# Kernel tuning notes

Hardware: AMD Instinct MI355X
Metric: run time of the kernel (lower is better)

Reference implementation:

```python
import jax, jax.numpy as jnp
import numpy as np

B = 2
SP = (480, 360, 32)   # spatial_shape (z, y, x)
GS = (8, 8, 8)        # query_gs_ratio
EP = (40, 15, 16)     # embed_params (pool compress ratio)
H = 8
N = 120000
D = 256
OUT = 20


def _dims(rat):
    return tuple((s + r - 1) // r for s, r in zip(SP, rat))


def sine_pe(coords, d_pos):
    # coords: [M,3] float voxel coords in original grid units; normalized sine PE
    nf = d_pos // 6
    sp = jnp.asarray(SP, jnp.float32)
    cn = coords / sp * (2.0 * jnp.pi)                      # normalize=True
    t = 10000.0 ** (jnp.arange(nf, dtype=jnp.float32) / nf)
    ang = cn[:, :, None] / t                               # [M,3,nf]
    pe = jnp.concatenate([jnp.sin(ang), jnp.cos(ang)], -1).reshape(coords.shape[0], -1)
    return jnp.pad(pe, ((0, 0), (0, d_pos - 6 * nf)))


def setup_inputs() -> dict:
    key = jax.random.key(0)
    ks = jax.random.split(key, 24)
    idx_b = jax.random.randint(ks[0], (N, 1), 0, B)
    idx_z = jax.random.randint(ks[1], (N, 1), 0, SP[0])
    idx_y = jax.random.randint(ks[2], (N, 1), 0, SP[1])
    idx_x = jax.random.randint(ks[3], (N, 1), 0, SP[2])
    indices = jnp.concatenate([idx_b, idx_z, idx_y, idx_x], axis=1).astype(jnp.int32)
    s = D ** -0.5
    p = lambda k, sh: jax.random.normal(k, sh, jnp.float32) * s
    return {
        'features': jax.random.normal(ks[4], (N, D), jnp.float32),
        'W_pool': p(ks[5], (D, D)), 'b_pool': jnp.zeros((D,), jnp.float32),
        'W_emb': p(ks[6], (D, D)), 'b_emb': jnp.zeros((D,), jnp.float32),
        'Wq': p(ks[7], (D, D)), 'bq': jnp.zeros((D,), jnp.float32),
        'Wk': p(ks[8], (D, D)), 'bk': jnp.zeros((D,), jnp.float32),
        'Wv': p(ks[9], (D, D)), 'bv': jnp.zeros((D,), jnp.float32),
        'Wo': p(ks[10], (D, D)), 'bo': jnp.zeros((D,), jnp.float32),
        'ln_g': jnp.ones((D,), jnp.float32), 'ln_b': jnp.zeros((D,), jnp.float32),
        'W_seg': p(ks[11], (D, OUT)), 'b_seg': jnp.zeros((OUT,), jnp.float32),
        'indices': indices,
        'batch_size': B,
    }


def reference(features, W_pool, b_pool, W_emb, b_emb, Wq, bq, Wk, bk, Wv, bv,
              Wo, bo, ln_g, ln_b, W_seg, b_seg, indices, batch_size):
    Zd, Yd, Xd = _dims(GS)
    Gq = Zd * Yd * Xd
    Sq = batch_size * Gq
    Ze, Ye, Xe = _dims(EP)
    Gk = Ze * Ye * Xe
    Sk = batch_size * Gk
    n = features.shape[0]

    # --- query pool branch: linear -> voxel-grid scatter_max ---
    pf = features @ W_pool + b_pool                                    # [N,D]
    dq = indices[:, 1:] // jnp.asarray(GS, jnp.int32)
    seg_q = ((indices[:, 0] * Zd + dq[:, 0]) * Yd + dq[:, 1]) * Xd + dq[:, 2]
    pool_max = jax.ops.segment_max(pf, seg_q, num_segments=Sq)
    cnt_q = jax.ops.segment_sum(jnp.ones((n,), jnp.float32), seg_q, num_segments=Sq)
    mq = cnt_q > 0
    pool_max = jnp.where(mq[:, None], pool_max, 0.0)
    cell = jnp.arange(Sq)
    rem = cell % Gq
    pool_c = jnp.stack([(rem // (Yd * Xd)) * GS[0],
                        ((rem // Xd) % Yd) * GS[1],
                        (rem % Xd) * GS[2]], -1).astype(jnp.float32)   # [Sq,3]

    # --- embedding branch ('pool'): linear -> coarse scatter_max + per-channel argmax coords ---
    ef = features @ W_emb + b_emb                                      # [N,D]
    de = indices[:, 1:] // jnp.asarray(EP, jnp.int32)
    seg_k = ((indices[:, 0] * Ze + de[:, 0]) * Ye + de[:, 1]) * Xe + de[:, 2]
    emb_max = jax.ops.segment_max(ef, seg_k, num_segments=Sk)
    cnt_k = jax.ops.segment_sum(jnp.ones((n,), jnp.float32), seg_k, num_segments=Sk)
    mk = cnt_k > 0
    emb_max = jnp.where(mk[:, None], emb_max, 0.0)
    winner = ef == jnp.where(mk[:, None], emb_max, -jnp.inf)[seg_k]
    idx = jax.ops.segment_max(jnp.where(winner, jnp.arange(n)[:, None], -1), seg_k, num_segments=Sk)
    idx_c = jnp.clip(idx, 0, n - 1)                                    # [Sk,D]
    ec = de.astype(jnp.float32)                                        # [N,3] downsampled coords
    emb_c = ec[idx_c].mean(axis=1) * jnp.asarray(EP, jnp.float32)      # [Sk,3]

    # --- position encoding (pointwise sine PE; per-batch loop in torch is pointwise-equivalent) ---
    pool_max = pool_max + sine_pe(pool_c, D)
    emb_max = emb_max + sine_pe(emb_c, D)

    # --- multi-head cross-attention (Q=pool, K/V=embedding), per-batch via dense grid reshape ---
    q_in = pool_max.reshape(batch_size, Gq, D)
    kv_in = emb_max.reshape(batch_size, Gk, D)
    dh = D // H
    q = (q_in @ Wq + bq).reshape(batch_size, Gq, H, dh)
    k = (kv_in @ Wk + bk).reshape(batch_size, Gk, H, dh)
    v = (kv_in @ Wv + bv).reshape(batch_size, Gk, H, dh)
    scores = jnp.einsum('bqhd,bkhd->bhqk', q, k) / jnp.float32(dh) ** 0.5
    kmask = mk.reshape(batch_size, Gk)
    scores = jnp.where(kmask[:, None, None, :], scores, -1e9)
    attn = jax.nn.softmax(scores, axis=-1)
    o = jnp.einsum('bhqk,bkhd->bqhd', attn, v).reshape(batch_size, Gq, D) @ Wo + bo
    h = q_in + o                                                       # residual + LayerNorm sublayer
    mu = h.mean(-1, keepdims=True)
    var = h.var(-1, keepdims=True)
    h = (h - mu) * jax.lax.rsqrt(var + 1e-5) * ln_g + ln_b
    feats_mhca = h.reshape(Sq, D)

    # --- gather back to voxels via pool_inv, residual, seg head (center-tap of SubMConv3d) ---
    vox = features + feats_mhca[seg_q]
    logits = vox @ W_seg + b_seg
    return logits
```

## Files before the change

### kernel.cpp

```cpp
#include <hip/hip_runtime.h>
#include <math.h>

#define N_PTS 120000
#define D 256
#define BATCH 2
#define NH 8
#define DH 32
#define OUTC 20

#define Zd 60
#define Yd 45
#define Xd 4
#define Gq 10800
#define Sq 21600

#define Ze 12
#define Ye 24
#define Xe 2
#define Gk 576
#define Sk 1152

typedef __bf16 bf16_t;
typedef __attribute__((ext_vector_type(8))) __bf16 bf16x8;
typedef __attribute__((ext_vector_type(4))) __bf16 bf16x4;
typedef __attribute__((ext_vector_type(4))) float f32x4;

__device__ __forceinline__ void glds16(const void* g, void* l) {
    __builtin_amdgcn_global_load_lds(
        (const __attribute__((address_space(1))) unsigned int*)g,
        (__attribute__((address_space(3))) unsigned int*)l,
        16, 0, 0);
}

__global__ __launch_bounds__(256) void k_prep(
    const float* __restrict__ Wp, const float* __restrict__ We,
    const float* __restrict__ Wq, const float* __restrict__ Wk,
    const float* __restrict__ Wv, const float* __restrict__ Wo,
    const float* __restrict__ bp, const float* __restrict__ be,
    const float* __restrict__ bk, const float* __restrict__ bv,
    const float* __restrict__ Wseg, const float* __restrict__ bseg,
    bf16_t* __restrict__ Wpe, bf16_t* __restrict__ Wqt,
    bf16_t* __restrict__ Wkv, bf16_t* __restrict__ Wot,
    bf16_t* __restrict__ Wsegt,
    float* __restrict__ bpe, float* __restrict__ bkv,
    float* __restrict__ bsegp)
{
    int n = blockIdx.x, k = threadIdx.x;
    if (n < 512) {
        const float* S = (n < 256) ? Wp : We;
        int nn = n & 255;
        Wpe[n * 256 + k] = (bf16_t)S[k * 256 + nn];
    } else if (n < 768) {
        int nn = n - 512;
        Wqt[nn * 256 + k] = (bf16_t)Wq[k * 256 + nn];
    } else if (n < 1280) {
        int m2 = n - 768;
        const float* S = (m2 < 256) ? Wk : Wv;
        int nn = m2 & 255;
        Wkv[m2 * 256 + k] = (bf16_t)S[k * 256 + nn];
    } else if (n < 1536) {
        int nn = n - 1280;
        Wot[nn * 256 + k] = (bf16_t)Wo[k * 256 + nn];
    } else if (n == 1536) {
        bpe[k] = bp[k]; bpe[256 + k] = be[k];
        bkv[k] = bk[k]; bkv[256 + k] = bv[k];
        if (k < 32) bsegp[k] = (k < OUTC) ? bseg[k] : 0.f;
    } else {
        int n2 = n - 1537;
        Wsegt[n2 * 256 + k] = (n2 < OUTC) ? (bf16_t)Wseg[k * OUTC + n2] : (bf16_t)0.f;
    }
}

__global__ __launch_bounds__(256) void k_cast(
    const float* __restrict__ in, bf16_t* __restrict__ out)
{
    const size_t total = (size_t)N_PTS * 32;
    const size_t stride = (size_t)gridDim.x * 256;
    for (size_t i = (size_t)blockIdx.x * 256 + threadIdx.x; i < total; i += stride) {
        float4 a = *(const float4*)(in + i * 8);
        float4 b = *(const float4*)(in + i * 8 + 4);
        bf16x8 o;
        o[0] = (bf16_t)a.x; o[1] = (bf16_t)a.y; o[2] = (bf16_t)a.z; o[3] = (bf16_t)a.w;
        o[4] = (bf16_t)b.x; o[5] = (bf16_t)b.y; o[6] = (bf16_t)b.z; o[7] = (bf16_t)b.w;
        *(bf16x8*)(out + i * 8) = o;
    }
}

__global__ __launch_bounds__(256) void k_count(
    const int* __restrict__ indices, int* __restrict__ cnt_q, int* __restrict__ cnt_k,
    int* __restrict__ segq, int* __restrict__ segk)
{
    int i = blockIdx.x * 256 + threadIdx.x;
    if (i >= N_PTS) return;
    const int* id = indices + (size_t)i * 4;
    int b = id[0], z = id[1], y = id[2], x = id[3];
    int sq = ((b * Zd + (z >> 3)) * Yd + (y >> 3)) * Xd + (x >> 3);
    int sk = ((b * Ze + (z / 40)) * Ye + (y / 15)) * Xe + (x >> 4);
    segq[i] = sq; segk[i] = sk;
    atomicAdd(&cnt_q[sq], 1);
    atomicAdd(&cnt_k[sk], 1);
}

__global__ __launch_bounds__(1024) void k_scan(
    const int* __restrict__ cnt, int n, int* __restrict__ offs, int* __restrict__ cursor)
{
    __shared__ int wbase[17];
    __shared__ int carry_s;
    const int t = threadIdx.x, lane = t & 63, w = t >> 6;
    if (t == 0) carry_s = 0;
    __syncthreads();
    for (int base = 0; base < n; base += 1024) {
        int v = (base + t < n) ? cnt[base + t] : 0;
        int incl = v;
        #pragma unroll
        for (int off = 1; off < 64; off <<= 1) {
            int u = __shfl_up(incl, off);
            if (lane >= off) incl += u;
        }
        if (lane == 63) wbase[w + 1] = incl;
        __syncthreads();
        if (t == 0) {
            int s = 0;
            wbase[0] = 0;
            #pragma unroll
            for (int i = 1; i <= 16; ++i) { s += wbase[i]; wbase[i] = s; }
        }
        __syncthreads();
        int excl = incl - v + wbase[w] + carry_s;
        if (base + t < n) { offs[base + t] = excl; cursor[base + t] = excl; }
        __syncthreads();
        if (t == 0) carry_s += wbase[16];
        __syncthreads();
    }
}

__global__ __launch_bounds__(256) void k_place(
    const int* __restrict__ segq, const int* __restrict__ segk,
    int* __restrict__ cur_q, int* __restrict__ cur_k,
    int* __restrict__ ids_q, int* __restrict__ ids_k)
{
    int i = blockIdx.x * 256 + threadIdx.x;
    if (i >= N_PTS) return;
    ids_q[atomicAdd(&cur_q[segq[i]], 1)] = i;
    ids_k[atomicAdd(&cur_k[segk[i]], 1)] = i;
}

__global__ __launch_bounds__(256) void k_gemm_bf(
    const bf16_t* __restrict__ A, int M,
    const bf16_t* __restrict__ Wt, const float* __restrict__ bias,
    bf16_t* __restrict__ outb, int ldo)
{
    __shared__ __align__(16) bf16_t Abuf[128 * 64];
    __shared__ __align__(16) bf16_t Bbuf[128 * 64];

    const int t = threadIdx.x;
    const int wave = t >> 6, lane = t & 63;
    const int wr = wave >> 1, wc = wave & 1;
    const int lrow = lane & 15, quad = lane >> 4;
    const int lr8 = lane >> 3, lc8 = lane & 7;
    const int row0 = blockIdx.y * 128;
    const int ntile = blockIdx.x;

    f32x4 acc[4][4];
    #pragma unroll
    for (int mi = 0; mi < 4; ++mi)
        #pragma unroll
        for (int ni = 0; ni < 4; ++ni)
            acc[mi][ni] = (f32x4){0.f, 0.f, 0.f, 0.f};

    for (int k0 = 0; k0 < 256; k0 += 64) {
        #pragma unroll
        for (int i = 0; i < 4; ++i) {
            int chunk = wave * 4 + i;
            int rowA = row0 + chunk * 8 + lr8;
            if (rowA > M - 1) rowA = M - 1;
            glds16(A + (size_t)rowA * 256 + k0 + lc8 * 8, &Abuf[chunk * 512]);
        }
        #pragma unroll
        for (int i = 0; i < 4; ++i) {
            int chunk = wave * 4 + i;
            glds16(Wt + (size_t)(ntile * 128 + chunk * 8 + lr8) * 256 + k0 + lc8 * 8,
                   &Bbuf[chunk * 512]);
        }
        asm volatile("s_waitcnt vmcnt(0)" ::: "memory");
        __builtin_amdgcn_sched_barrier(0);
        __syncthreads();

        #pragma unroll
        for (int kk = 0; kk < 64; kk += 32) {
            bf16x8 Af[4], Bf[4];
            #pragma unroll
            for (int mi = 0; mi < 4; ++mi)
                Af[mi] = *(const bf16x8*)&Abuf[(wr * 64 + mi * 16 + lrow) * 64 + kk + quad * 8];
            #pragma unroll
            for (int ni = 0; ni < 4; ++ni)
                Bf[ni] = *(const bf16x8*)&Bbuf[(wc * 64 + ni * 16 + lrow) * 64 + kk + quad * 8];
            #pragma unroll
            for (int mi = 0; mi < 4; ++mi)
                #pragma unroll
                for (int ni = 0; ni < 4; ++ni)
                    acc[mi][ni] = __builtin_amdgcn_mfma_f32_16x16x32_bf16(
                        Af[mi], Bf[ni], acc[mi][ni], 0, 0, 0);
        }
        __syncthreads();
    }

    const int colb = ntile * 128 + wc * 64;
    float biasv[4];
    #pragma unroll
    for (int ni = 0; ni < 4; ++ni) biasv[ni] = bias[colb + ni * 16 + lrow];

    #pragma unroll
    for (int mi = 0; mi < 4; ++mi) {
        int lr = wr * 64 + mi * 16 + quad * 4;
        #pragma unroll
        for (int reg = 0; reg < 4; ++reg) {
            int grow = row0 + lr + reg;
            if (grow >= M) continue;
            #pragma unroll
            for (int ni = 0; ni < 4; ++ni) {
                int col = colb + ni * 16 + lrow;
                outb[(size_t)grow * ldo + col] = (bf16_t)(acc[mi][ni][reg] + biasv[ni]);
            }
        }
    }
}

__global__ __launch_bounds__(512, 2) void k_gemm(
    const float* __restrict__ A, int M,
    const bf16_t* __restrict__ Wt, const float* __restrict__ bias,
    int mode, float* __restrict__ outp, int ldo)
{
    __shared__ __align__(16) bf16_t Abuf[128][72];
    __shared__ __align__(16) bf16_t Bbuf[256][72];

    const int t = threadIdx.x;
    const int wave = t >> 6, lane = t & 63;
    const int wr = wave >> 2, wc = wave & 3;
    const int lrow = lane & 15, quad = lane >> 4;
    const int row0 = blockIdx.y * 128;
    const int ntile = blockIdx.x;

    f32x4 acc[4][4];
    #pragma unroll
    for (int mi = 0; mi < 4; ++mi)
        #pragma unroll
        for (int ni = 0; ni < 4; ++ni)
            acc[mi][ni] = (f32x4){0.f, 0.f, 0.f, 0.f};

    for (int k0 = 0; k0 < 256; k0 += 64) {
        #pragma unroll
        for (int i = 0; i < 4; ++i) {
            int c = i * 512 + t;
            int r = c >> 4, c4 = c & 15;
            float4 v = make_float4(0.f, 0.f, 0.f, 0.f);
            if (row0 + r < M)
                v = *(const float4*)(A + (size_t)(row0 + r) * 256 + k0 + c4 * 4);
            bf16x4 bv4;
            bv4[0] = (bf16_t)v.x; bv4[1] = (bf16_t)v.y;
            bv4[2] = (bf16_t)v.z; bv4[3] = (bf16_t)v.w;
            *(bf16x4*)&Abuf[r][c4 * 4] = bv4;
        }
        #pragma unroll
        for (int i = 0; i < 4; ++i) {
            int c = i * 512 + t;
            int r = c >> 3, c8 = c & 7;
            uint4 w = *(const uint4*)(Wt + ((size_t)(ntile * 256 + r)) * 256 + k0 + c8 * 8);
            *(uint4*)&Bbuf[r][c8 * 8] = w;
        }
        __syncthreads();

        #pragma unroll
        for (int kk = 0; kk < 64; kk += 32) {
            bf16x8 Af[4], Bf[4];
            #pragma unroll
            for (int mi = 0; mi < 4; ++mi)
                Af[mi] = *(const bf16x8*)&Abuf[wr * 64 + mi * 16 + lrow][kk + quad * 8];
            #pragma unroll
            for (int ni = 0; ni < 4; ++ni)
                Bf[ni] = *(const bf16x8*)&Bbuf[wc * 64 + ni * 16 + lrow][kk + quad * 8];
            #pragma unroll
            for (int mi = 0; mi < 4; ++mi)
                #pragma unroll
                for (int ni = 0; ni < 4; ++ni)
                    acc[mi][ni] = __builtin_amdgcn_mfma_f32_16x16x32_bf16(
                        Af[mi], Bf[ni], acc[mi][ni], 0, 0, 0);
        }
        __syncthreads();
    }

    const int colb = ntile * 256 + wc * 64;
    float biasv[4];
    #pragma unroll
    for (int ni = 0; ni < 4; ++ni) biasv[ni] = bias[colb + ni * 16 + lrow];

    if (mode == 0) {
        #pragma unroll
        for (int mi = 0; mi < 4; ++mi) {
            int lr = wr * 64 + mi * 16 + quad * 4;
            #pragma unroll
            for (int reg = 0; reg < 4; ++reg) {
                int grow = row0 + lr + reg;
                if (grow >= M) continue;
                #pragma unroll
                for (int ni = 0; ni < 4; ++ni) {
                    int col = colb + ni * 16 + lrow;
                    outp[(size_t)grow * ldo + col] = acc[mi][ni][reg] + biasv[ni];
                }
            }
        }
    } else {
        bf16_t* outb = (bf16_t*)outp;
        #pragma unroll
        for (int mi = 0; mi < 4; ++mi) {
            int lr = wr * 64 + mi * 16 + quad * 4;
            #pragma unroll
            for (int reg = 0; reg < 4; ++reg) {
                int grow = row0 + lr + reg;
                if (grow >= M) continue;
                #pragma unroll
                for (int ni = 0; ni < 4; ++ni) {
                    int col = colb + ni * 16 + lrow;
                    outb[(size_t)grow * ldo + col] = (bf16_t)(acc[mi][ni][reg] + biasv[ni]);
                }
            }
        }
    }
}

__device__ inline float pe_val(int j, float cz, float cy, float cx) {
    if (j >= 252) return 0.f;
    int dim = j / 84;
    int f = j % 84;
    int fi = (f >= 42) ? (f - 42) : f;
    float c  = (dim == 0) ? cz : ((dim == 1) ? cy : cx);
    float sp = (dim == 0) ? 480.f : ((dim == 1) ? 360.f : 32.f);
    float cn = c / sp * 6.28318530717958647692f;
    float tt = expf((float)fi * (9.210340371976184f / 42.f));
    float ang = cn / tt;
    return (f >= 42) ? cosf(ang) : sinf(ang);
}

__global__ __launch_bounds__(256) void k_pool_q(
    const bf16_t* __restrict__ pfb, const int* __restrict__ ids,
    const int* __restrict__ offs, const int* __restrict__ cnt,
    float* __restrict__ out)
{
    const int t = threadIdx.x, lane = t & 63, w = t >> 6;
    const int s = blockIdx.x * 4 + w;
    if (s >= Sq) return;
    const int count = cnt[s], start = offs[s];
    float mx[4] = {-3.0e38f, -3.0e38f, -3.0e38f, -3.0e38f};
    for (int r = 0; r < count; ++r) {
        int i = ids[start + r];
        bf16x4 v = *(const bf16x4*)(pfb + (size_t)i * 256 + lane * 4);
        #pragma unroll
        for (int j = 0; j < 4; ++j) mx[j] = fmaxf(mx[j], (float)v[j]);
    }
    int rem = s % Gq;
    float cz = (float)((rem / (Yd * Xd)) * 8);
    float cy = (float)(((rem / Xd) % Yd) * 8);
    float cx = (float)((rem % Xd) * 8);
    #pragma unroll
    for (int j = 0; j < 4; ++j) {
        float v = (count > 0) ? mx[j] : 0.f;
        out[(size_t)s * 256 + lane * 4 + j] = v + pe_val(lane * 4 + j, cz, cy, cx);
    }
}

__global__ __launch_bounds__(512) void k_pool_k(
    const bf16_t* __restrict__ efb, const int* __restrict__ ids,
    const int* __restrict__ offs, const int* __restrict__ cnt,
    float* __restrict__ out, int* __restrict__ kmask)
{
    __shared__ float red[8][256];
    const int t = threadIdx.x, lane = t & 63, w = t >> 6;
    const int s = blockIdx.x;
    const int count = cnt[s], start = offs[s];
    float mx[4] = {-3.0e38f, -3.0e38f, -3.0e38f, -3.0e38f};
    for (int r = w; r < count; r += 8) {
        int i = ids[start + r];
        bf16x4 v = *(const bf16x4*)(efb + (size_t)i * 256 + lane * 4);
        #pragma unroll
        for (int j = 0; j < 4; ++j) mx[j] = fmaxf(mx[j], (float)v[j]);
    }
    #pragma unroll
    for (int j = 0; j < 4; ++j) red[w][lane * 4 + j] = mx[j];
    __syncthreads();
    if (t < 256) {
        float m = red[0][t];
        #pragma unroll
        for (int i = 1; i < 8; ++i) m = fmaxf(m, red[i][t]);
        if (count == 0) m = 0.f;
        int rem = s % Gk;
        float cz = (float)((rem / (Ye * Xe)) * 40);
        float cy = (float)(((rem / Xe) % Ye) * 15);
        float cx = (float)((rem % Xe) * 16);
        out[(size_t)s * 256 + t] = m + pe_val(t, cz, cy, cx);
        if (t == 0) kmask[s] = (count > 0) ? 1 : 0;
    }
}

__global__ __launch_bounds__(256) void k_attn_mfma(
    const bf16_t* __restrict__ Q, const bf16_t* __restrict__ KV,
    const int* __restrict__ kmask, float* __restrict__ O)
{
    __shared__ __align__(16) bf16_t Qs[64][40];
    __shared__ __align__(16) bf16_t Ks[192][40];
    __shared__ __align__(16) bf16_t Vts[32][200];
    __shared__ __align__(16) bf16_t Ps[4][16][200];
    __shared__ float mskf[192];

    const int bh = blockIdx.y;
    const int b = bh >> 3, h = bh & 7;
    const int t = threadIdx.x, wave = t >> 6, lane = t & 63;
    const int lrow = lane & 15, quad = lane >> 4;
    const int q0 = blockIdx.x * 64;

    {
        int r = t >> 2, part = t & 3;
        int qi = q0 + r;
        uint4 val = make_uint4(0u, 0u, 0u, 0u);
        if (qi < Gq)
            val = *(const uint4*)(Q + ((size_t)(b * Gq + qi)) * 256 + h * 32 + part * 8);
        *(uint4*)&Qs[r][part * 8] = val;
    }
    __syncthreads();

    const bf16x8 Aq = *(const bf16x8*)&Qs[wave * 16 + lrow][quad * 8];

    f32x4 oacc[2];
    oacc[0] = (f32x4){0.f, 0.f, 0.f, 0.f};
    oacc[1] = (f32x4){0.f, 0.f, 0.f, 0.f};
    float m_run[4], l_run[4];
    #pragma unroll
    for (int r = 0; r < 4; ++r) { m_run[r] = -3.0e38f; l_run[r] = 0.f; }

    for (int c0 = 0; c0 < Gk; c0 += 192) {
        __syncthreads();
        #pragma unroll
        for (int i = 0; i < 3; ++i) {
            int idx = i * 256 + t;
            int kk = idx >> 2, part = idx & 3;
            uint4 val = *(const uint4*)(KV + ((size_t)(b * Gk + c0 + kk)) * 512 + h * 32 + part * 8);
            *(uint4*)&Ks[kk][part * 8] = val;
        }
        #pragma unroll
        for (int i = 0; i < 3; ++i) {
            int idx = i * 256 + t;
            int kk = idx >> 2, part = idx & 3;
            bf16x8 v = *(const bf16x8*)(KV + ((size_t)(b * Gk + c0 + kk)) * 512 + 256 + h * 32 + part * 8);
            #pragma unroll
            for (int j = 0; j < 8; ++j)
                Vts[part * 8 + j][kk] = v[j];
        }
        if (t < 192) mskf[t] = kmask[b * Gk + c0 + t] ? 0.f : -1.0e9f;
        __syncthreads();

        float sreg[12][4];
        #pragma unroll
        for (int nt = 0; nt < 12; ++nt) {
            bf16x8 Bk = *(const bf16x8*)&Ks[nt * 16 + lrow][quad * 8];
            f32x4 sacc = __builtin_amdgcn_mfma_f32_16x16x32_bf16(
                Aq, Bk, (f32x4){0.f, 0.f, 0.f, 0.f}, 0, 0, 0);
            float pen = mskf[nt * 16 + lrow];
            #pragma unroll
            for (int r = 0; r < 4; ++r)
                sreg[nt][r] = sacc[r] * 0.17677669529663688f + pen;
        }

        float alpha[4];
        #pragma unroll
        for (int r = 0; r < 4; ++r) {
            float mx = sreg[0][r];
            #pragma unroll
            for (int nt = 1; nt < 12; ++nt) mx = fmaxf(mx, sreg[nt][r]);
            #pragma unroll
            for (int off = 1; off < 16; off <<= 1)
                mx = fmaxf(mx, __shfl_xor(mx, off));
            float mnew = fmaxf(m_run[r], mx);
            alpha[r] = __expf(m_run[r] - mnew);
            m_run[r] = mnew;
            l_run[r] *= alpha[r];
        }
        #pragma unroll
        for (int n2 = 0; n2 < 2; ++n2)
            #pragma unroll
            for (int r = 0; r < 4; ++r) oacc[n2][r] *= alpha[r];

        float psum[4] = {0.f, 0.f, 0.f, 0.f};
        #pragma unroll
        for (int nt = 0; nt < 12; ++nt) {
            #pragma unroll
            for (int r = 0; r < 4; ++r) {
                float p = __expf(sreg[nt][r] - m_run[r]);
                psum[r] += p;
                Ps[wave][quad * 4 + r][nt * 16 + lrow] = (bf16_t)p;
            }
        }
        #pragma unroll
        for (int r = 0; r < 4; ++r) {
            float s = psum[r];
            #pragma unroll
            for (int off = 1; off < 16; off <<= 1) s += __shfl_xor(s, off);
            l_run[r] += s;
        }

        #pragma unroll
        for (int ks = 0; ks < 6; ++ks) {
            bf16x8 Ap = *(const bf16x8*)&Ps[wave][lrow][ks * 32 + quad * 8];
            #pragma unroll
            for (int n2 = 0; n2 < 2; ++n2) {
                bf16x8 Bv = *(const bf16x8*)&Vts[n2 * 16 + lrow][ks * 32 + quad * 8];
                oacc[n2] = __builtin_amdgcn_mfma_f32_16x16x32_bf16(
                    Ap, Bv, oacc[n2], 0, 0, 0);
            }
        }
    }

    #pragma unroll
    for (int r = 0; r < 4; ++r) {
        int qi = q0 + wave * 16 + quad * 4 + r;
        if (qi >= Gq) continue;
        float inv = (l_run[r] > 0.f) ? (1.f / l_run[r]) : 0.f;
        #pragma unroll
        for (int n2 = 0; n2 < 2; ++n2)
            O[((size_t)(b * Gq + qi)) * 256 + h * 32 + n2 * 16 + lrow] = oacc[n2][r] * inv;
    }
}

__global__ __launch_bounds__(256) void k_ln(
    const float* __restrict__ oproj, const float* __restrict__ resid,
    const float* __restrict__ g, const float* __restrict__ bta,
    float* __restrict__ out)
{
    const int s = blockIdx.x, t = threadIdx.x;
    float h = resid[(size_t)s * D + t] + oproj[(size_t)s * D + t];

    float s1 = h, s2 = h * h;
    for (int o = 32; o > 0; o >>= 1) {
        s1 += __shfl_down(s1, o);
        s2 += __shfl_down(s2, o);
    }
    __shared__ float r1[4], r2[4];
    __shared__ float mu_s, rstd_s;
    int w = t >> 6;
    if ((t & 63) == 0) { r1[w] = s1; r2[w] = s2; }
    __syncthreads();
    if (t == 0) {
        float a = r1[0] + r1[1] + r1[2] + r1[3];
        float bsum = r2[0] + r2[1] + r2[2] + r2[3];
        float mu = a * (1.f / 256.f);
        float var = bsum * (1.f / 256.f) - mu * mu;
        mu_s = mu;
        rstd_s = rsqrtf(var + 1e-5f);
    }
    __syncthreads();
    out[(size_t)s * D + t] = (h - mu_s) * rstd_s * g[t] + bta[t];
}

__global__ __launch_bounds__(512, 2) void k_logits_mfma(
    const float* __restrict__ feat, const float* __restrict__ mhca,
    const int* __restrict__ indices, const bf16_t* __restrict__ Wsegt,
    const float* __restrict__ bsegp, float* __restrict__ out)
{
    __shared__ __align__(16) bf16_t Abuf[128][72];
    __shared__ __align__(16) bf16_t Bbuf[32][72];
    __shared__ int sq_s[128];

    const int t = threadIdx.x;
    const int wave = t >> 6, lane = t & 63;
    const int lrow = lane & 15, quad = lane >> 4;
    const int row0 = blockIdx.x * 128;

    if (t < 128) {
        int row = row0 + t;
        if (row < N_PTS) {
            const int* id = indices + (size_t)row * 4;
            sq_s[t] = ((id[0] * Zd + (id[1] >> 3)) * Yd + (id[2] >> 3)) * Xd + (id[3] >> 3);
        } else sq_s[t] = 0;
    }
    __syncthreads();

    f32x4 acc[2];
    acc[0] = (f32x4){0.f, 0.f, 0.f, 0.f};
    acc[1] = (f32x4){0.f, 0.f, 0.f, 0.f};

    for (int k0 = 0; k0 < 256; k0 += 64) {
        #pragma unroll
        for (int i = 0; i < 4; ++i) {
            int c = i * 512 + t;
            int r = c >> 4, c4 = c & 15;
            float4 v = make_float4(0.f, 0.f, 0.f, 0.f);
            int grow = row0 + r;
            if (grow < N_PTS) {
                v = *(const float4*)(feat + (size_t)grow * 256 + k0 + c4 * 4);
                float4 m = *(const float4*)(mhca + (size_t)sq_s[r] * 256 + k0 + c4 * 4);
                v.x += m.x; v.y += m.y; v.z += m.z; v.w += m.w;
            }
            bf16x4 bv4;
            bv4[0] = (bf16_t)v.x; bv4[1] = (bf16_t)v.y;
            bv4[2] = (bf16_t)v.z; bv4[3] = (bf16_t)v.w;
            *(bf16x4*)&Abuf[r][c4 * 4] = bv4;
        }
        if (t < 256) {
            int r = t >> 3, c8 = t & 7;
            uint4 w = *(const uint4*)(Wsegt + (size_t)r * 256 + k0 + c8 * 8);
            *(uint4*)&Bbuf[r][c8 * 8] = w;
        }
        __syncthreads();

        #pragma unroll
        for (int kk = 0; kk < 64; kk += 32) {
            bf16x8 Af = *(const bf16x8*)&Abuf[wave * 16 + lrow][kk + quad * 8];
            #pragma unroll
            for (int ni = 0; ni < 2; ++ni) {
                bf16x8 Bf = *(const bf16x8*)&Bbuf[ni * 16 + lrow][kk + quad * 8];
                acc[ni] = __builtin_amdgcn_mfma_f32_16x16x32_bf16(
                    Af, Bf, acc[ni], 0, 0, 0);
            }
        }
        __syncthreads();
    }

    #pragma unroll
    for (int ni = 0; ni < 2; ++ni) {
        int col = ni * 16 + lrow;
        if (col >= OUTC) continue;
        float bias = bsegp[col];
        #pragma unroll
        for (int reg = 0; reg < 4; ++reg) {
            int grow = row0 + wave * 16 + quad * 4 + reg;
            if (grow >= N_PTS) continue;
            out[(size_t)grow * OUTC + col] = acc[ni][reg] + bias;
        }
    }
}

extern "C" void kernel_launch(void* const* d_in, const int* in_sizes, int n_in,
                              void* d_out, int out_size, void* d_ws, size_t ws_size,
                              hipStream_t stream) {
    const float* features = (const float*)d_in[0];
    const float* W_pool = (const float*)d_in[1];
    const float* b_pool = (const float*)d_in[2];
    const float* W_emb  = (const float*)d_in[3];
    const float* b_emb  = (const float*)d_in[4];
    const float* Wq = (const float*)d_in[5];
    const float* bq = (const float*)d_in[6];
    const float* Wk = (const float*)d_in[7];
    const float* bk = (const float*)d_in[8];
    const float* Wv = (const float*)d_in[9];
    const float* bv = (const float*)d_in[10];
    const float* Wo = (const float*)d_in[11];
    const float* bo = (const float*)d_in[12];
    const float* ln_g = (const float*)d_in[13];
    const float* ln_b = (const float*)d_in[14];
    const float* W_seg = (const float*)d_in[15];
    const float* b_seg = (const float*)d_in[16];
    const int* indices = (const int*)d_in[17];
    float* out = (float*)d_out;

    float* ws = (float*)d_ws;
    const size_t SQD = (size_t)Sq * D;
    const size_t SKD = (size_t)Sk * D;
    const size_t PFB_FL = (size_t)N_PTS * D / 2;

    size_t oP   = 0;
    size_t oPF  = oP + PFB_FL;
    size_t oEF  = oPF + SQD;
    size_t oWpe = oEF + SKD;
    size_t oWqt = oWpe + 65536;
    size_t oWkv = oWqt + 32768;
    size_t oWot = oWkv + 65536;
    size_t obpe = oWot + 32768;
    size_t obkv = obpe + 512;
    size_t oCnt = obkv + 512;
    size_t oOffq = oCnt + 21600 + 1152;
    size_t oCurq = oOffq + 21600;
    size_t oOffk = oCurq + 21600;
    size_t oCurk = oOffk + 1152;
    size_t oSegq = oCurk + 1152;
    size_t oSegk = oSegq + N_PTS;
    size_t oIdsq = oSegk + N_PTS;
    size_t oIdsk = oIdsq + N_PTS;
    size_t oKm   = oIdsk + N_PTS;
    size_t oWst  = oKm + 1152;
    size_t obsg  = oWst + 4096;
    size_t oFB   = obsg + 32;

    bf16_t* pfb = (bf16_t*)(ws + oP);
    float* pool_feat = ws + oPF;
    float* emb_feat  = ws + oEF;
    bf16_t* Wpe = (bf16_t*)(ws + oWpe);
    bf16_t* Wqt = (bf16_t*)(ws + oWqt);
    bf16_t* Wkv = (bf16_t*)(ws + oWkv);
    bf16_t* Wot = (bf16_t*)(ws + oWot);
    float* bpe = ws + obpe;
    float* bkv = ws + obkv;
    int* cnt_q = (int*)(ws + oCnt);
    int* cnt_k = cnt_q + 21600;
    int* offs_q = (int*)(ws + oOffq);
    int* cur_q  = (int*)(ws + oCurq);
    int* offs_k = (int*)(ws + oOffk);
    int* cur_k  = (int*)(ws + oCurk);
    int* segq = (int*)(ws + oSegq);
    int* segk = (int*)(ws + oSegk);
    int* ids_q = (int*)(ws + oIdsq);
    int* ids_k = (int*)(ws + oIdsk);
    int* kmask = (int*)(ws + oKm);
    bf16_t* Wsegt = (bf16_t*)(ws + oWst);
    float* bsegp = ws + obsg;
    bf16_t* fb16 = (bf16_t*)(ws + oFB);

    bf16_t* Qb  = (bf16_t*)(ws + oP);
    bf16_t* KVb = (bf16_t*)(ws + oP + 2764800);
    float* attnO = ws + oP + 3059712;
    float* oproj = ws + oP + 8589312;
    float* mhca  = ws + oP + 3059712;

    const bool fast = ws_size >= (oFB + PFB_FL) * sizeof(float);

    hipMemsetAsync(cnt_q, 0, (21600 + 1152) * sizeof(int), stream);

    k_prep<<<1569, 256, 0, stream>>>(W_pool, W_emb, Wq, Wk, Wv, Wo,
                                     b_pool, b_emb, bk, bv, W_seg, b_seg,
                                     Wpe, Wqt, Wkv, Wot, Wsegt, bpe, bkv, bsegp);

    if (fast)
        k_cast<<<2048, 256, 0, stream>>>(features, fb16);

    k_count<<<(N_PTS + 255) / 256, 256, 0, stream>>>(indices, cnt_q, cnt_k, segq, segk);
    k_scan<<<1, 1024, 0, stream>>>(cnt_q, 21600, offs_q, cur_q);
    k_scan<<<1, 1024, 0, stream>>>(cnt_k, 1152, offs_k, cur_k);
    k_place<<<(N_PTS + 255) / 256, 256, 0, stream>>>(segq, segk, cur_q, cur_k, ids_q, ids_k);

    if (fast) {
        dim3 g(2, (N_PTS + 127) / 128);
        k_gemm_bf<<<g, 256, 0, stream>>>(fb16, N_PTS, Wpe + 256 * 256, bpe + 256,
                                         pfb, 256);
    } else {
        dim3 g(1, (N_PTS + 127) / 128);
        k_gemm<<<g, 512, 0, stream>>>(features, N_PTS, Wpe + 256 * 256, bpe + 256, 2,
                                      (float*)pfb, 256);
    }
    k_pool_k<<<Sk, 512, 0, stream>>>(pfb, ids_k, offs_k, cnt_k, emb_feat, kmask);

    if (fast) {
        dim3 g(2, (N_PTS + 127) / 128);
        k_gemm_bf<<<g, 256, 0, stream>>>(fb16, N_PTS, Wpe, bpe, pfb, 256);
    } else {
        dim3 g(1, (N_PTS + 127) / 128);
        k_gemm<<<g, 512, 0, stream>>>(features, N_PTS, Wpe, bpe, 2,
                                      (float*)pfb, 256);
    }
    k_pool_q<<<(Sq + 3) / 4, 256, 0, stream>>>(pfb, ids_q, offs_q, cnt_q, pool_feat);

    {
        dim3 g(1, (Sq + 127) / 128);
        k_gemm<<<g, 512, 0, stream>>>(pool_feat, Sq, Wqt, bq, 2, (float*)Qb, 256);
    }
    {
        dim3 g(2, (Sk + 127) / 128);
        k_gemm<<<g, 512, 0, stream>>>(emb_feat, Sk, Wkv, bkv, 2, (float*)KVb, 512);
    }

    {
        dim3 ag((Gq + 63) / 64, BATCH * NH);
        k_attn_mfma<<<ag, 256, 0, stream>>>(Qb, KVb, kmask, attnO);
    }

    {
        dim3 g(1, (Sq + 127) / 128);
        k_gemm<<<g, 512, 0, stream>>>(attnO, Sq, Wot, bo, 0, oproj, 256);
    }

    k_ln<<<Sq, 256, 0, stream>>>(oproj, pool_feat, ln_g, ln_b, mhca);

    k_logits_mfma<<<(N_PTS + 127) / 128, 512, 0, stream>>>(
        features, mhca, indices, Wsegt, bsegp, out);
}
```

Before: 594.2 us.

## Restructure attention to stage full K/V per block with pre-transposed V

Adds a kernel that writes V transposed into a separate buffer. The attention kernel now uses 768-thread blocks covering 192 queries and loads all 576 keys and the transposed V into shared memory once, so the per-chunk reloads and the scalar LDS transpose of V go away. Q is read straight from global memory, and the mask is stored as bf16. It also raises the occupancy hint on the bf16 GEMM. The trade-offs are more shared memory per block, fewer and larger blocks, and one extra launch plus a workspace buffer that reuses the emb_feat region, which must still be safe to overwrite at that point.

Measured after the change: 600.1 us. Within noise of the previous version (+1.0%).

```diff
diff --git a/kernel.cpp b/kernel.cpp
--- a/kernel.cpp
+++ b/kernel.cpp
@@ -145,7 +145,7 @@
     ids_k[atomicAdd(&cur_k[segk[i]], 1)] = i;
 }
 
-__global__ __launch_bounds__(256) void k_gemm_bf(
+__global__ __launch_bounds__(256, 4) void k_gemm_bf(
     const bf16_t* __restrict__ A, int M,
     const bf16_t* __restrict__ Wt, const float* __restrict__ bias,
     bf16_t* __restrict__ outb, int ldo)
@@ -401,33 +401,55 @@
     }
 }
 
-__global__ __launch_bounds__(256) void k_attn_mfma(
+__global__ __launch_bounds__(256) void k_vt(
+    const bf16_t* __restrict__ KVb, bf16_t* __restrict__ VT)
+{
+    int idx = blockIdx.x * 256 + threadIdx.x;
+    if (idx >= 16 * 32 * 576) return;
+    int g = idx % 576;
+    int d = (idx / 576) & 31;
+    int bh = idx / (576 * 32);
+    int b = bh >> 3, h = bh & 7;
+    VT[idx] = KVb[((size_t)(b * Gk + g)) * 512 + 256 + h * 32 + d];
+}
+
+__global__ __launch_bounds__(768, 3) void k_attn2(
     const bf16_t* __restrict__ Q, const bf16_t* __restrict__ KV,
-    const int* __restrict__ kmask, float* __restrict__ O)
-{
-    __shared__ __align__(16) bf16_t Qs[64][40];
-    __shared__ __align__(16) bf16_t Ks[192][40];
-    __shared__ __align__(16) bf16_t Vts[32][200];
-    __shared__ __align__(16) bf16_t Ps[4][16][200];
-    __shared__ float mskf[192];
+    const bf16_t* __restrict__ VT, const int* __restrict__ kmask,
+    float* __restrict__ O)
+{
+    __shared__ __align__(16) bf16_t Ks[576][40];
+    __shared__ __align__(16) bf16_t Vts[32][584];
+    __shared__ __align__(16) bf16_t Ps[12][16][104];
+    __shared__ bf16_t mskb[576];
 
     const int bh = blockIdx.y;
     const int b = bh >> 3, h = bh & 7;
     const int t = threadIdx.x, wave = t >> 6, lane = t & 63;
     const int lrow = lane & 15, quad = lane >> 4;
-    const int q0 = blockIdx.x * 64;
-
-    {
-        int r = t >> 2, part = t & 3;
-        int qi = q0 + r;
-        uint4 val = make_uint4(0u, 0u, 0u, 0u);
-        if (qi < Gq)
-            val = *(const uint4*)(Q + ((size_t)(b * Gq + qi)) * 256 + h * 32 + part * 8);
-        *(uint4*)&Qs[r][part * 8] = val;
-    }
+    const int q0 = blockIdx.x * 192;
+
+    #pragma unroll
+    for (int i = 0; i < 3; ++i) {
+        int id = i * 768 + t;
+        int kk = id >> 2, part = id & 3;
+        uint4 v = *(const uint4*)(KV + ((size_t)(b * Gk + kk)) * 512 + h * 32 + part * 8);
+        *(uint4*)&Ks[kk][part * 8] = v;
+    }
+    #pragma unroll
+    for (int i = 0; i < 3; ++i) {
+        int id = i * 768 + t;
+        int d = id / 72, c8 = id % 72;
+        uint4 v = *(const uint4*)(VT + (size_t)(bh * 32 + d) * 576 + c8 * 8);
+        *(uint4*)&Vts[d][c8 * 8] = v;
+    }
+    if (t < 576)
+        mskb[t] = kmask[b * Gk + t] ? (bf16_t)0.f : (bf16_t)(-1.0e9f);
     __syncthreads();
 
-    const bf16x8 Aq = *(const bf16x8*)&Qs[wave * 16 + lrow][quad * 8];
+    int qa = q0 + wave * 16 + lrow;
+    if (qa > Gq - 1) qa = Gq - 1;
+    const bf16x8 Aq = *(const bf16x8*)(Q + ((size_t)(b * Gq + qa)) * 256 + h * 32 + quad * 8);
 
     f32x4 oacc[2];
     oacc[0] = (f32x4){0.f, 0.f, 0.f, 0.f};
@@ -436,34 +458,14 @@
     #pragma unroll
     for (int r = 0; r < 4; ++r) { m_run[r] = -3.0e38f; l_run[r] = 0.f; }
 
-    for (int c0 = 0; c0 < Gk; c0 += 192) {
-        __syncthreads();
-        #pragma unroll
-        for (int i = 0; i < 3; ++i) {
-            int idx = i * 256 + t;
-            int kk = idx >> 2, part = idx & 3;
-            uint4 val = *(const uint4*)(KV + ((size_t)(b * Gk + c0 + kk)) * 512 + h * 32 + part * 8);
-            *(uint4*)&Ks[kk][part * 8] = val;
-        }
-        #pragma unroll
-        for (int i = 0; i < 3; ++i) {
-            int idx = i * 256 + t;
-            int kk = idx >> 2, part = idx & 3;
-            bf16x8 v = *(const bf16x8*)(KV + ((size_t)(b * Gk + c0 + kk)) * 512 + 256 + h * 32 + part * 8);
-            #pragma unroll
-            for (int j = 0; j < 8; ++j)
-                Vts[part * 8 + j][kk] = v[j];
-        }
-        if (t < 192) mskf[t] = kmask[b * Gk + c0 + t] ? 0.f : -1.0e9f;
-        __syncthreads();
-
-        float sreg[12][4];
-        #pragma unroll
-        for (int nt = 0; nt < 12; ++nt) {
-            bf16x8 Bk = *(const bf16x8*)&Ks[nt * 16 + lrow][quad * 8];
+    for (int c0 = 0; c0 < Gk; c0 += 96) {
+        float sreg[6][4];
+        #pragma unroll
+        for (int nt = 0; nt < 6; ++nt) {
+            bf16x8 Bk = *(const bf16x8*)&Ks[c0 + nt * 16 + lrow][quad * 8];
             f32x4 sacc = __builtin_amdgcn_mfma_f32_16x16x32_bf16(
                 Aq, Bk, (f32x4){0.f, 0.f, 0.f, 0.f}, 0, 0, 0);
-            float pen = mskf[nt * 16 + lrow];
+            float pen = (float)mskb[c0 + nt * 16 + lrow];
             #pragma unroll
             for (int r = 0; r < 4; ++r)
                 sreg[nt][r] = sacc[r] * 0.17677669529663688f + pen;
@@ -474,7 +476,7 @@
         for (int r = 0; r < 4; ++r) {
             float mx = sreg[0][r];
             #pragma unroll
-            for (int nt = 1; nt < 12; ++nt) mx = fmaxf(mx, sreg[nt][r]);
+            for (int nt = 1; nt < 6; ++nt) mx = fmaxf(mx, sreg[nt][r]);
             #pragma unroll
             for (int off = 1; off < 16; off <<= 1)
                 mx = fmaxf(mx, __shfl_xor(mx, off));
@@ -490,7 +492,7 @@
 
         float psum[4] = {0.f, 0.f, 0.f, 0.f};
         #pragma unroll
-        for (int nt = 0; nt < 12; ++nt) {
+        for (int nt = 0; nt < 6; ++nt) {
             #pragma unroll
             for (int r = 0; r < 4; ++r) {
                 float p = __expf(sreg[nt][r] - m_run[r]);
@@ -507,11 +509,11 @@
         }
 
         #pragma unroll
-        for (int ks = 0; ks < 6; ++ks) {
+        for (int ks = 0; ks < 3; ++ks) {
             bf16x8 Ap = *(const bf16x8*)&Ps[wave][lrow][ks * 32 + quad * 8];
             #pragma unroll
             for (int n2 = 0; n2 < 2; ++n2) {
-                bf16x8 Bv = *(const bf16x8*)&Vts[n2 * 16 + lrow][ks * 32 + quad * 8];
+                bf16x8 Bv = *(const bf16x8*)&Vts[n2 * 16 + lrow][c0 + ks * 32 + quad * 8];
                 oacc[n2] = __builtin_amdgcn_mfma_f32_16x16x32_bf16(
                     Ap, Bv, oacc[n2], 0, 0, 0);
             }
@@ -717,6 +719,7 @@
     float* attnO = ws + oP + 3059712;
     float* oproj = ws + oP + 8589312;
     float* mhca  = ws + oP + 3059712;
+    bf16_t* VT = (bf16_t*)(ws + oEF);
 
     const bool fast = ws_size >= (oFB + PFB_FL) * sizeof(float);
 
@@ -764,9 +767,11 @@
         k_gemm<<<g, 512, 0, stream>>>(emb_feat, Sk, Wkv, bkv, 2, (float*)KVb, 512);
     }
 
+    k_vt<<<(16 * 32 * 576 + 255) / 256, 256, 0, stream>>>(KVb, VT);
+
     {
-        dim3 ag((Gq + 63) / 64, BATCH * NH);
-        k_attn_mfma<<<ag, 256, 0, stream>>>(Qb, KVb, kmask, attnO);
+        dim3 ag((Gq + 191) / 192, BATCH * NH);
+        k_attn2<<<ag, 768, 0, stream>>>(Qb, KVb, VT, kmask, attnO);
     }
 
     {
```
